# Kernel tuning notes

Hardware: AMD Instinct MI355X
Metric: run time of the kernel (lower is better)

Reference implementation:

```python
import jax, jax.numpy as jnp
import numpy as np

N, E = 50000, 800000
IN, HID, OUT, T = 96, 128, 64, 8
THETA = 0.5


def setup_inputs() -> dict:
    key = jax.random.key(0)
    ks = jax.random.split(key, 8)
    x = jax.random.normal(ks[0], (N, IN), dtype=jnp.float32)
    edge_weight = jax.random.uniform(ks[1], (E,), dtype=jnp.float32)
    W1 = jax.random.normal(ks[2], (IN, HID), dtype=jnp.float32) * (2.0 / np.sqrt(IN + HID))
    W2 = jax.random.normal(ks[3], (HID, OUT), dtype=jnp.float32) * (2.0 / np.sqrt(HID + OUT))
    # Bernoulli(1 - theta) masks, fixed per MC sample (created in __init__)
    mask1 = (jax.random.uniform(ks[4], (T, IN, HID)) < (1.0 - THETA)).astype(jnp.float32)
    mask2 = (jax.random.uniform(ks[5], (T, HID, OUT)) < (1.0 - THETA)).astype(jnp.float32)
    src = jax.random.randint(ks[6], (E,), 0, N, dtype=jnp.int32)
    dst = jax.random.randint(ks[7], (E,), 0, N, dtype=jnp.int32)
    return {"x": x, "edge_weight": edge_weight, "W1": W1, "W2": W2,
            "mask1": mask1, "mask2": mask2, "src": src, "dst": dst}


def _spmm(feat, edge_weight, src, dst, n_nodes):
    # u_mul_e('feat','edge_weight') followed by fn.sum onto dst nodes
    msg = feat[src] * edge_weight[:, None]          # [E, D]
    return jax.ops.segment_sum(msg, dst, num_segments=n_nodes)  # [N, D]


def reference(x, edge_weight, W1, W2, mask1, mask2, src, dst):
    n = x.shape[0]
    # first aggregation is mask-independent -> compute once, share across T samples
    agg1 = _spmm(x, edge_weight, src, dst, n)       # [N, IN]

    def per_sample(m1, m2):
        h = jax.nn.relu(agg1 @ (W1 * m1))           # [N, HID]
        agg2 = _spmm(h, edge_weight, src, dst, n)   # [N, HID]
        return agg2 @ (W2 * m2)                     # [N, OUT]

    # stack of the T per-sample outputs (torch version returns a list)
    return jax.vmap(per_sample)(mask1, mask2)       # [T, N, OUT]
```

## Files before the change

### kernel.cpp

```cpp
#include <hip/hip_runtime.h>

#define N_NODES 50000
#define N_EDGES 800000
#define IN_F 96
#define HID_F 128
#define OUT_F 64
#define T_S 8
#define CAP 48

#define NB_ZERO 196
#define NB_XB 4688
#define NB_WPREP 640
#define NB_PREP (NB_ZERO + NB_XB + NB_WPREP)

typedef __attribute__((ext_vector_type(8))) short short8;
typedef __attribute__((ext_vector_type(4))) float float4v;
typedef __attribute__((ext_vector_type(2))) unsigned uint2v;
typedef __attribute__((ext_vector_type(4))) unsigned uint4v;

__device__ __forceinline__ float bf2f(unsigned short h) {
    unsigned u = ((unsigned)h) << 16;
    float f;
    __builtin_memcpy(&f, &u, 4);
    return f;
}
__device__ __forceinline__ unsigned short f2bf(float f) {
    unsigned u;
    __builtin_memcpy(&u, &f, 4);
    unsigned r = (u + 0x7fffu + ((u >> 16) & 1u)) >> 16;
    return (unsigned short)r;
}
__device__ __forceinline__ float bf_lo(unsigned u) {
    unsigned v = u << 16;
    float f;
    __builtin_memcpy(&f, &v, 4);
    return f;
}
__device__ __forceinline__ float bf_hi(unsigned u) {
    unsigned v = u & 0xffff0000u;
    float f;
    __builtin_memcpy(&f, &v, 4);
    return f;
}

__global__ __launch_bounds__(256) void k_prep(int* __restrict__ cursor,
                                              const float* __restrict__ x,
                                              unsigned short* __restrict__ xb,
                                              const float* __restrict__ W1,
                                              const float* __restrict__ W2,
                                              const float* __restrict__ m1,
                                              const float* __restrict__ m2,
                                              unsigned short* __restrict__ wf) {
    int bid = blockIdx.x;
    if (bid < NB_ZERO) {
        int i = bid * 256 + threadIdx.x;
        if (i < N_NODES) cursor[i] = 0;
        return;
    }
    bid -= NB_ZERO;
    if (bid < NB_XB) {
        int i = bid * 256 + threadIdx.x;
        int idx = i * 4;
        if (idx < N_NODES * IN_F) {
            float4v v = __builtin_nontemporal_load((const float4v*)(x + idx));
            uint2v r;
            r.x = (unsigned)f2bf(v.x) | ((unsigned)f2bf(v.y) << 16);
            r.y = (unsigned)f2bf(v.z) | ((unsigned)f2bf(v.w) << 16);
            *(uint2v*)(xb + idx) = r;
        }
        return;
    }
    bid -= NB_XB;
    {
        int gid = bid * 256 + threadIdx.x;
        if (gid >= T_S * 20480) return;
        int t = gid / 20480;
        int idx = gid % 20480;
        float val;
        if (idx < 12288) {
            int j = idx & 7, lane = (idx >> 3) & 63, fr = idx >> 9;
            int kk = fr >> 3, nt = fr & 7;
            int k = kk * 32 + (lane >> 4) * 8 + j;
            int n = nt * 16 + (lane & 15);
            val = W1[k * HID_F + n] * m1[((size_t)t * IN_F + k) * HID_F + n];
        } else {
            int i2 = idx - 12288;
            int j = i2 & 7, lane = (i2 >> 3) & 63, fr = i2 >> 9;
            int kk = fr >> 2, ot = fr & 3;
            int k = kk * 32 + (lane >> 4) * 8 + j;
            int o = ot * 16 + (lane & 15);
            val = W2[k * OUT_F + o] * m2[((size_t)t * HID_F + k) * OUT_F + o];
        }
        wf[gid] = f2bf(val);
    }
}

__global__ void k_fillB(const int* __restrict__ src, const int* __restrict__ dst,
                        const float* __restrict__ ew, int* __restrict__ cursor,
                        uint2v* __restrict__ bucket) {
    int e = blockIdx.x * 256 + threadIdx.x;
    if (e < N_EDGES) {
        int d = dst[e];
        int pos = atomicAdd(&cursor[d], 1);
        if (pos < CAP) {
            uint2v c;
            c.x = (unsigned)src[e];
            c.y = __float_as_uint(ew[e]);
            __builtin_nontemporal_store(c, &bucket[(size_t)d * CAP + pos]);
        }
    }
}

__global__ __launch_bounds__(256) void k_spmm1(const unsigned short* __restrict__ xb,
                                               const int* __restrict__ cursor,
                                               const uint2v* __restrict__ bucket,
                                               unsigned short* __restrict__ agg1) {
    int wave = threadIdx.x >> 6, lane = threadIdx.x & 63;
    int node = blockIdx.x * 4 + wave;
    int g = lane >> 4, d = lane & 15;
    int dd = (d < 12) ? d : 0;
    int cnt = cursor[node];
    if (cnt > CAP) cnt = CAP;
    int beg = node * CAP, end = beg + cnt;
    const uint4v* xrow = (const uint4v*)xb;
    float acc[8] = {0.f, 0.f, 0.f, 0.f, 0.f, 0.f, 0.f, 0.f};
    int e = beg;
    for (; e + 15 < end; e += 16) {
        uint2v c[4];
        uint4v dt[4];
#pragma unroll
        for (int i = 0; i < 4; i++) c[i] = bucket[e + i * 4 + g];
#pragma unroll
        for (int i = 0; i < 4; i++) dt[i] = xrow[(size_t)c[i].x * 12 + dd];
#pragma unroll
        for (int i = 0; i < 4; i++) {
            float wv = __uint_as_float(c[i].y);
            acc[0] = fmaf(wv, bf_lo(dt[i].x), acc[0]);
            acc[1] = fmaf(wv, bf_hi(dt[i].x), acc[1]);
            acc[2] = fmaf(wv, bf_lo(dt[i].y), acc[2]);
            acc[3] = fmaf(wv, bf_hi(dt[i].y), acc[3]);
            acc[4] = fmaf(wv, bf_lo(dt[i].z), acc[4]);
            acc[5] = fmaf(wv, bf_hi(dt[i].z), acc[5]);
            acc[6] = fmaf(wv, bf_lo(dt[i].w), acc[6]);
            acc[7] = fmaf(wv, bf_hi(dt[i].w), acc[7]);
        }
    }
    for (; e < end; e += 4) {
        int ee = e + g;
        bool ea = ee < end;
        uint2v c = bucket[ea ? ee : beg];
        float wv = ea ? __uint_as_float(c.y) : 0.f;
        uint4v dt = xrow[(size_t)c.x * 12 + dd];
        acc[0] = fmaf(wv, bf_lo(dt.x), acc[0]);
        acc[1] = fmaf(wv, bf_hi(dt.x), acc[1]);
        acc[2] = fmaf(wv, bf_lo(dt.y), acc[2]);
        acc[3] = fmaf(wv, bf_hi(dt.y), acc[3]);
        acc[4] = fmaf(wv, bf_lo(dt.z), acc[4]);
        acc[5] = fmaf(wv, bf_hi(dt.z), acc[5]);
        acc[6] = fmaf(wv, bf_lo(dt.w), acc[6]);
        acc[7] = fmaf(wv, bf_hi(dt.w), acc[7]);
    }
#pragma unroll
    for (int j = 0; j < 8; j++) {
        acc[j] += __shfl_xor(acc[j], 16);
        acc[j] += __shfl_xor(acc[j], 32);
    }
    if (lane < 12) {
        uint4v pk;
        pk.x = (unsigned)f2bf(acc[0]) | ((unsigned)f2bf(acc[1]) << 16);
        pk.y = (unsigned)f2bf(acc[2]) | ((unsigned)f2bf(acc[3]) << 16);
        pk.z = (unsigned)f2bf(acc[4]) | ((unsigned)f2bf(acc[5]) << 16);
        pk.w = (unsigned)f2bf(acc[6]) | ((unsigned)f2bf(acc[7]) << 16);
        ((uint4v*)agg1)[(size_t)node * 12 + d] = pk;
    }
}

__global__ __launch_bounds__(256) void k_gemm(const unsigned short* __restrict__ agg1,
                                              const unsigned short* __restrict__ wfrags,
                                              unsigned short* __restrict__ P, int tBase,
                                              int nodeStride, int tMul) {
    __shared__ __align__(16) unsigned short ldsW[20480];
    __shared__ __align__(16) unsigned short ldsH[4][2176];
    int t = tBase + blockIdx.y;
    const uint4* wsrc = (const uint4*)(wfrags + (size_t)t * 20480);
    uint4* wdst = (uint4*)ldsW;
    for (int i = threadIdx.x; i < 2560; i += 256) wdst[i] = wsrc[i];
    __syncthreads();

    int wave = threadIdx.x >> 6, lane = threadIdx.x & 63;
    int quad = lane >> 4, l15 = lane & 15;

    for (int it = 0; it < 8; it++) {
        int node = blockIdx.x * 512 + it * 64 + wave * 16 + l15;
        bool v = node < N_NODES;

        short8 a[3];
        if (v) {
            const unsigned short* ap = agg1 + (size_t)node * IN_F;
            a[0] = *(const short8*)(ap + 0 * 32 + quad * 8);
            a[1] = *(const short8*)(ap + 1 * 32 + quad * 8);
            a[2] = *(const short8*)(ap + 2 * 32 + quad * 8);
        } else {
            short8 z = {0, 0, 0, 0, 0, 0, 0, 0};
            a[0] = z; a[1] = z; a[2] = z;
        }

        for (int nt = 0; nt < 8; nt++) {
            float4v acc = {0.f, 0.f, 0.f, 0.f};
            for (int kk = 0; kk < 3; kk++) {
                short8 w = *(const short8*)&ldsW[(kk * 8 + nt) * 512 + lane * 8];
                acc = __builtin_amdgcn_mfma_f32_16x16x32_bf16(w, a[kk], acc, 0, 0, 0);
            }
            unsigned h0 = f2bf(fmaxf(acc[0], 0.f));
            unsigned h1 = f2bf(fmaxf(acc[1], 0.f));
            unsigned h2 = f2bf(fmaxf(acc[2], 0.f));
            unsigned h3 = f2bf(fmaxf(acc[3], 0.f));
            uint2 pk;
            pk.x = h0 | (h1 << 16);
            pk.y = h2 | (h3 << 16);
            *(uint2*)&ldsH[wave][l15 * 136 + nt * 16 + quad * 4] = pk;
        }

        short8 hf[4];
        for (int kk = 0; kk < 4; kk++)
            hf[kk] = *(const short8*)&ldsH[wave][l15 * 136 + kk * 32 + quad * 8];

        unsigned short* Pt = P + (size_t)node * nodeStride + (size_t)t * tMul;
        for (int ot = 0; ot < 4; ot++) {
            float4v acc = {0.f, 0.f, 0.f, 0.f};
            for (int kk = 0; kk < 4; kk++) {
                short8 w = *(const short8*)&ldsW[12288 + (kk * 4 + ot) * 512 + lane * 8];
                acc = __builtin_amdgcn_mfma_f32_16x16x32_bf16(w, hf[kk], acc, 0, 0, 0);
            }
            if (v) {
                uint2 pk;
                pk.x = (unsigned)f2bf(acc[0]) | ((unsigned)f2bf(acc[1]) << 16);
                pk.y = (unsigned)f2bf(acc[2]) | ((unsigned)f2bf(acc[3]) << 16);
                *(uint2*)(Pt + ot * 16 + quad * 4) = pk;
            }
        }
    }
}

__global__ __launch_bounds__(256) void k_spmm2(const unsigned short* __restrict__ P,
                                               const int* __restrict__ cursor,
                                               const uint2v* __restrict__ bucket,
                                               float* __restrict__ out) {
    int wave = threadIdx.x >> 6, lane = threadIdx.x & 63;
    int node = blockIdx.x * 4 + wave;
    int cnt = cursor[node];
    if (cnt > CAP) cnt = CAP;
    int beg = node * CAP, end = beg + cnt;
    const uint4v* Pl = (const uint4v*)P + lane;
    float acc[8] = {0.f, 0.f, 0.f, 0.f, 0.f, 0.f, 0.f, 0.f};
    int e = beg;
    for (; e + 7 < end; e += 8) {
        uint2v c[8];
        uint4v d[8];
#pragma unroll
        for (int i = 0; i < 8; i++) c[i] = bucket[e + i];
#pragma unroll
        for (int i = 0; i < 8; i++) d[i] = Pl[(size_t)c[i].x * 64];
#pragma unroll
        for (int i = 0; i < 8; i++) {
            float wv = __uint_as_float(c[i].y);
            acc[0] = fmaf(wv, bf_lo(d[i].x), acc[0]);
            acc[1] = fmaf(wv, bf_hi(d[i].x), acc[1]);
            acc[2] = fmaf(wv, bf_lo(d[i].y), acc[2]);
            acc[3] = fmaf(wv, bf_hi(d[i].y), acc[3]);
            acc[4] = fmaf(wv, bf_lo(d[i].z), acc[4]);
            acc[5] = fmaf(wv, bf_hi(d[i].z), acc[5]);
            acc[6] = fmaf(wv, bf_lo(d[i].w), acc[6]);
            acc[7] = fmaf(wv, bf_hi(d[i].w), acc[7]);
        }
    }
    for (; e + 3 < end; e += 4) {
        uint2v c[4];
        uint4v d[4];
#pragma unroll
        for (int i = 0; i < 4; i++) c[i] = bucket[e + i];
#pragma unroll
        for (int i = 0; i < 4; i++) d[i] = Pl[(size_t)c[i].x * 64];
#pragma unroll
        for (int i = 0; i < 4; i++) {
            float wv = __uint_as_float(c[i].y);
            acc[0] = fmaf(wv, bf_lo(d[i].x), acc[0]);
            acc[1] = fmaf(wv, bf_hi(d[i].x), acc[1]);
            acc[2] = fmaf(wv, bf_lo(d[i].y), acc[2]);
            acc[3] = fmaf(wv, bf_hi(d[i].y), acc[3]);
            acc[4] = fmaf(wv, bf_lo(d[i].z), acc[4]);
            acc[5] = fmaf(wv, bf_hi(d[i].z), acc[5]);
            acc[6] = fmaf(wv, bf_lo(d[i].w), acc[6]);
            acc[7] = fmaf(wv, bf_hi(d[i].w), acc[7]);
        }
    }
    for (; e < end; e++) {
        uint2v c = bucket[e];
        float wv = __uint_as_float(c.y);
        uint4v d = Pl[(size_t)c.x * 64];
        acc[0] = fmaf(wv, bf_lo(d.x), acc[0]);
        acc[1] = fmaf(wv, bf_hi(d.x), acc[1]);
        acc[2] = fmaf(wv, bf_lo(d.y), acc[2]);
        acc[3] = fmaf(wv, bf_hi(d.y), acc[3]);
        acc[4] = fmaf(wv, bf_lo(d.z), acc[4]);
        acc[5] = fmaf(wv, bf_hi(d.z), acc[5]);
        acc[6] = fmaf(wv, bf_lo(d.w), acc[6]);
        acc[7] = fmaf(wv, bf_hi(d.w), acc[7]);
    }
    int t = lane >> 3, o = (lane & 7) * 8;
    float* op = out + ((size_t)t * N_NODES + node) * OUT_F + o;
    float4v v0 = {acc[0], acc[1], acc[2], acc[3]};
    float4v v1 = {acc[4], acc[5], acc[6], acc[7]};
    *(float4v*)op = v0;
    *(float4v*)(op + 4) = v1;
}

__global__ __launch_bounds__(512) void k_spmm2_1t(const unsigned short* __restrict__ P,
                                                  const int* __restrict__ cursor,
                                                  const uint2v* __restrict__ bucket,
                                                  float* __restrict__ out) {
    int node = blockIdx.x * 8 + (threadIdx.x >> 6);
    int o = threadIdx.x & 63;
    if (node >= N_NODES) return;
    int cnt = cursor[node];
    if (cnt > CAP) cnt = CAP;
    int beg = node * CAP, end = beg + cnt;
    const unsigned short* Pt = P + o;
    float a0 = 0.f, a1 = 0.f, a2 = 0.f, a3 = 0.f;
    int e = beg;
    for (; e + 3 < end; e += 4) {
        uint2v c0 = bucket[e];
        uint2v c1 = bucket[e + 1];
        uint2v c2 = bucket[e + 2];
        uint2v c3 = bucket[e + 3];
        a0 += __uint_as_float(c0.y) * bf2f(Pt[(size_t)c0.x * OUT_F]);
        a1 += __uint_as_float(c1.y) * bf2f(Pt[(size_t)c1.x * OUT_F]);
        a2 += __uint_as_float(c2.y) * bf2f(Pt[(size_t)c2.x * OUT_F]);
        a3 += __uint_as_float(c3.y) * bf2f(Pt[(size_t)c3.x * OUT_F]);
    }
    for (; e < end; e++) {
        uint2v c = bucket[e];
        a0 += __uint_as_float(c.y) * bf2f(Pt[(size_t)c.x * OUT_F]);
    }
    out[(size_t)node * OUT_F + o] = a0 + a1 + a2 + a3;
}

extern "C" void kernel_launch(void* const* d_in, const int* in_sizes, int n_in,
                              void* d_out, int out_size, void* d_ws, size_t ws_size,
                              hipStream_t stream) {
    const float* x = (const float*)d_in[0];
    const float* ew = (const float*)d_in[1];
    const float* W1 = (const float*)d_in[2];
    const float* W2 = (const float*)d_in[3];
    const float* m1 = (const float*)d_in[4];
    const float* m2 = (const float*)d_in[5];
    const int* src = (const int*)d_in[6];
    const int* dst = (const int*)d_in[7];
    float* out = (float*)d_out;

    char* w = (char*)d_ws;
    size_t off = 0;
    auto alloc = [&](size_t bytes) -> void* {
        void* p = (void*)(w + off);
        off += (bytes + 255) & ~(size_t)255;
        return p;
    };
    int* cursor = (int*)alloc((size_t)N_NODES * 4);
    uint2v* bucket = (uint2v*)alloc((size_t)N_NODES * CAP * 8);
    unsigned short* agg1 = (unsigned short*)alloc((size_t)N_NODES * IN_F * 2);
    unsigned short* wf = (unsigned short*)alloc((size_t)T_S * 20480 * 2);

    size_t unionBase = off;
    size_t pBytesBatched = (size_t)T_S * N_NODES * OUT_F * 2;
    size_t xbBytes = (size_t)N_NODES * IN_F * 2;
    bool batched = ws_size >= unionBase + (pBytesBatched > xbBytes ? pBytesBatched : xbBytes);
    unsigned short* xb = (unsigned short*)(w + unionBase);
    unsigned short* P = (unsigned short*)(w + unionBase);
    if (!batched) {
        xb = (unsigned short*)(w + unionBase);
        P = (unsigned short*)(w + unionBase + ((xbBytes + 255) & ~(size_t)255));
    }

    k_prep<<<NB_PREP, 256, 0, stream>>>(cursor, x, xb, W1, W2, m1, m2, wf);
    k_fillB<<<N_EDGES / 256, 256, 0, stream>>>(src, dst, ew, cursor, bucket);
    k_spmm1<<<N_NODES / 4, 256, 0, stream>>>(xb, cursor, bucket, agg1);

    if (batched) {
        k_gemm<<<dim3(98, 8), 256, 0, stream>>>(agg1, wf, P, 0, T_S * OUT_F, OUT_F);
        k_spmm2<<<N_NODES / 4, 256, 0, stream>>>(P, cursor, bucket, out);
    } else {
        for (int t = 0; t < T_S; t++) {
            k_gemm<<<dim3(98, 1), 256, 0, stream>>>(agg1, wf, P, t, OUT_F, 0);
            k_spmm2_1t<<<6250, 512, 0, stream>>>(P, cursor, bucket,
                                                 out + (size_t)t * N_NODES * OUT_F);
        }
    }
}
```

Before: 362.7 us.

## Merge prep, bucket fill and first SpMM into one cooperative kernel

Replaces three separate launches (prep, edge bucketing, first aggregation) with a single cooperative kernel of 1024 persistent blocks that uses grid-wide syncs between phases and grid-stride loops. The aim is to remove launch gaps and tail effects between the three front-end stages. In exchange, phases now run on a fixed grid that may use the GPU less fully than the original large grids. Grid syncs add their own cost, and the cooperative launch requires all blocks to be co-resident.

```diff
diff --git a/kernel.cpp b/kernel.cpp
--- a/kernel.cpp
+++ b/kernel.cpp
@@ -1,4 +1,7 @@
 #include <hip/hip_runtime.h>
+#include <hip/hip_cooperative_groups.h>
+
+namespace cg = cooperative_groups;
 
 #define N_NODES 50000
 #define N_EDGES 800000
@@ -8,10 +11,9 @@
 #define T_S 8
 #define CAP 48
 
-#define NB_ZERO 196
-#define NB_XB 4688
-#define NB_WPREP 640
-#define NB_PREP (NB_ZERO + NB_XB + NB_WPREP)
+#define GRID_CO 1024
+#define NTH_CO (GRID_CO * 256)
+#define NWAVE_CO (GRID_CO * 4)
 
 typedef __attribute__((ext_vector_type(8))) short short8;
 typedef __attribute__((ext_vector_type(4))) float float4v;
@@ -43,39 +45,34 @@
     return f;
 }
 
-__global__ __launch_bounds__(256) void k_prep(int* __restrict__ cursor,
-                                              const float* __restrict__ x,
-                                              unsigned short* __restrict__ xb,
-                                              const float* __restrict__ W1,
-                                              const float* __restrict__ W2,
-                                              const float* __restrict__ m1,
-                                              const float* __restrict__ m2,
-                                              unsigned short* __restrict__ wf) {
-    int bid = blockIdx.x;
-    if (bid < NB_ZERO) {
-        int i = bid * 256 + threadIdx.x;
-        if (i < N_NODES) cursor[i] = 0;
-        return;
-    }
-    bid -= NB_ZERO;
-    if (bid < NB_XB) {
-        int i = bid * 256 + threadIdx.x;
+__global__ __launch_bounds__(256, 4) void k_front(int* __restrict__ cursor,
+                                                  const float* __restrict__ x,
+                                                  unsigned short* __restrict__ xb,
+                                                  const float* __restrict__ W1,
+                                                  const float* __restrict__ W2,
+                                                  const float* __restrict__ m1,
+                                                  const float* __restrict__ m2,
+                                                  unsigned short* __restrict__ wf,
+                                                  const int* __restrict__ src,
+                                                  const int* __restrict__ dst,
+                                                  const float* __restrict__ ew,
+                                                  uint2v* __restrict__ bucket,
+                                                  unsigned short* __restrict__ agg1) {
+    cg::grid_group grid = cg::this_grid();
+    int gtid = blockIdx.x * 256 + threadIdx.x;
+
+    if (gtid < N_NODES) cursor[gtid] = 0;
+    for (int i = gtid; i < N_NODES * IN_F / 4; i += NTH_CO) {
         int idx = i * 4;
-        if (idx < N_NODES * IN_F) {
-            float4v v = __builtin_nontemporal_load((const float4v*)(x + idx));
-            uint2v r;
-            r.x = (unsigned)f2bf(v.x) | ((unsigned)f2bf(v.y) << 16);
-            r.y = (unsigned)f2bf(v.z) | ((unsigned)f2bf(v.w) << 16);
-            *(uint2v*)(xb + idx) = r;
-        }
-        return;
-    }
-    bid -= NB_XB;
-    {
-        int gid = bid * 256 + threadIdx.x;
-        if (gid >= T_S * 20480) return;
-        int t = gid / 20480;
-        int idx = gid % 20480;
+        float4v v = __builtin_nontemporal_load((const float4v*)(x + idx));
+        uint2v r;
+        r.x = (unsigned)f2bf(v.x) | ((unsigned)f2bf(v.y) << 16);
+        r.y = (unsigned)f2bf(v.z) | ((unsigned)f2bf(v.w) << 16);
+        *(uint2v*)(xb + idx) = r;
+    }
+    if (gtid < T_S * 20480) {
+        int t = gtid / 20480;
+        int idx = gtid % 20480;
         float val;
         if (idx < 12288) {
             int j = idx & 7, lane = (idx >> 3) & 63, fr = idx >> 9;
@@ -91,15 +88,12 @@
             int o = ot * 16 + (lane & 15);
             val = W2[k * OUT_F + o] * m2[((size_t)t * HID_F + k) * OUT_F + o];
         }
-        wf[gid] = f2bf(val);
-    }
-}
-
-__global__ void k_fillB(const int* __restrict__ src, const int* __restrict__ dst,
-                        const float* __restrict__ ew, int* __restrict__ cursor,
-                        uint2v* __restrict__ bucket) {
-    int e = blockIdx.x * 256 + threadIdx.x;
-    if (e < N_EDGES) {
+        wf[gtid] = f2bf(val);
+    }
+
+    grid.sync();
+
+    for (int e = gtid; e < N_EDGES; e += NTH_CO) {
         int d = dst[e];
         int pos = atomicAdd(&cursor[d], 1);
         if (pos < CAP) {
@@ -109,69 +103,68 @@
             __builtin_nontemporal_store(c, &bucket[(size_t)d * CAP + pos]);
         }
     }
-}
-
-__global__ __launch_bounds__(256) void k_spmm1(const unsigned short* __restrict__ xb,
-                                               const int* __restrict__ cursor,
-                                               const uint2v* __restrict__ bucket,
-                                               unsigned short* __restrict__ agg1) {
-    int wave = threadIdx.x >> 6, lane = threadIdx.x & 63;
-    int node = blockIdx.x * 4 + wave;
+
+    grid.sync();
+
+    int lane = threadIdx.x & 63;
+    int gwave = gtid >> 6;
     int g = lane >> 4, d = lane & 15;
     int dd = (d < 12) ? d : 0;
-    int cnt = cursor[node];
-    if (cnt > CAP) cnt = CAP;
-    int beg = node * CAP, end = beg + cnt;
     const uint4v* xrow = (const uint4v*)xb;
-    float acc[8] = {0.f, 0.f, 0.f, 0.f, 0.f, 0.f, 0.f, 0.f};
-    int e = beg;
-    for (; e + 15 < end; e += 16) {
-        uint2v c[4];
-        uint4v dt[4];
-#pragma unroll
-        for (int i = 0; i < 4; i++) c[i] = bucket[e + i * 4 + g];
-#pragma unroll
-        for (int i = 0; i < 4; i++) dt[i] = xrow[(size_t)c[i].x * 12 + dd];
-#pragma unroll
-        for (int i = 0; i < 4; i++) {
-            float wv = __uint_as_float(c[i].y);
-            acc[0] = fmaf(wv, bf_lo(dt[i].x), acc[0]);
-            acc[1] = fmaf(wv, bf_hi(dt[i].x), acc[1]);
-            acc[2] = fmaf(wv, bf_lo(dt[i].y), acc[2]);
-            acc[3] = fmaf(wv, bf_hi(dt[i].y), acc[3]);
-            acc[4] = fmaf(wv, bf_lo(dt[i].z), acc[4]);
-            acc[5] = fmaf(wv, bf_hi(dt[i].z), acc[5]);
-            acc[6] = fmaf(wv, bf_lo(dt[i].w), acc[6]);
-            acc[7] = fmaf(wv, bf_hi(dt[i].w), acc[7]);
-        }
-    }
-    for (; e < end; e += 4) {
-        int ee = e + g;
-        bool ea = ee < end;
-        uint2v c = bucket[ea ? ee : beg];
-        float wv = ea ? __uint_as_float(c.y) : 0.f;
-        uint4v dt = xrow[(size_t)c.x * 12 + dd];
-        acc[0] = fmaf(wv, bf_lo(dt.x), acc[0]);
-        acc[1] = fmaf(wv, bf_hi(dt.x), acc[1]);
-        acc[2] = fmaf(wv, bf_lo(dt.y), acc[2]);
-        acc[3] = fmaf(wv, bf_hi(dt.y), acc[3]);
-        acc[4] = fmaf(wv, bf_lo(dt.z), acc[4]);
-        acc[5] = fmaf(wv, bf_hi(dt.z), acc[5]);
-        acc[6] = fmaf(wv, bf_lo(dt.w), acc[6]);
-        acc[7] = fmaf(wv, bf_hi(dt.w), acc[7]);
-    }
-#pragma unroll
-    for (int j = 0; j < 8; j++) {
-        acc[j] += __shfl_xor(acc[j], 16);
-        acc[j] += __shfl_xor(acc[j], 32);
-    }
-    if (lane < 12) {
-        uint4v pk;
-        pk.x = (unsigned)f2bf(acc[0]) | ((unsigned)f2bf(acc[1]) << 16);
-        pk.y = (unsigned)f2bf(acc[2]) | ((unsigned)f2bf(acc[3]) << 16);
-        pk.z = (unsigned)f2bf(acc[4]) | ((unsigned)f2bf(acc[5]) << 16);
-        pk.w = (unsigned)f2bf(acc[6]) | ((unsigned)f2bf(acc[7]) << 16);
-        ((uint4v*)agg1)[(size_t)node * 12 + d] = pk;
+    for (int node = gwave; node < N_NODES; node += NWAVE_CO) {
+        int cnt = cursor[node];
+        if (cnt > CAP) cnt = CAP;
+        int beg = node * CAP, end = beg + cnt;
+        float acc[8] = {0.f, 0.f, 0.f, 0.f, 0.f, 0.f, 0.f, 0.f};
+        int e = beg;
+        for (; e + 15 < end; e += 16) {
+            uint2v c[4];
+            uint4v dt[4];
+#pragma unroll
+            for (int i = 0; i < 4; i++) c[i] = bucket[e + i * 4 + g];
+#pragma unroll
+            for (int i = 0; i < 4; i++) dt[i] = xrow[(size_t)c[i].x * 12 + dd];
+#pragma unroll
+            for (int i = 0; i < 4; i++) {
+                float wv = __uint_as_float(c[i].y);
+                acc[0] = fmaf(wv, bf_lo(dt[i].x), acc[0]);
+                acc[1] = fmaf(wv, bf_hi(dt[i].x), acc[1]);
+                acc[2] = fmaf(wv, bf_lo(dt[i].y), acc[2]);
+                acc[3] = fmaf(wv, bf_hi(dt[i].y), acc[3]);
+                acc[4] = fmaf(wv, bf_lo(dt[i].z), acc[4]);
+                acc[5] = fmaf(wv, bf_hi(dt[i].z), acc[5]);
+                acc[6] = fmaf(wv, bf_lo(dt[i].w), acc[6]);
+                acc[7] = fmaf(wv, bf_hi(dt[i].w), acc[7]);
+            }
+        }
+        for (; e < end; e += 4) {
+            int ee = e + g;
+            bool ea = ee < end;
+            uint2v c = bucket[ea ? ee : beg];
+            float wv = ea ? __uint_as_float(c.y) : 0.f;
+            uint4v dt = xrow[(size_t)c.x * 12 + dd];
+            acc[0] = fmaf(wv, bf_lo(dt.x), acc[0]);
+            acc[1] = fmaf(wv, bf_hi(dt.x), acc[1]);
+            acc[2] = fmaf(wv, bf_lo(dt.y), acc[2]);
+            acc[3] = fmaf(wv, bf_hi(dt.y), acc[3]);
+            acc[4] = fmaf(wv, bf_lo(dt.z), acc[4]);
+            acc[5] = fmaf(wv, bf_hi(dt.z), acc[5]);
+            acc[6] = fmaf(wv, bf_lo(dt.w), acc[6]);
+            acc[7] = fmaf(wv, bf_hi(dt.w), acc[7]);
+        }
+#pragma unroll
+        for (int j = 0; j < 8; j++) {
+            acc[j] += __shfl_xor(acc[j], 16);
+            acc[j] += __shfl_xor(acc[j], 32);
+        }
+        if (lane < 12) {
+            uint4v pk;
+            pk.x = (unsigned)f2bf(acc[0]) | ((unsigned)f2bf(acc[1]) << 16);
+            pk.y = (unsigned)f2bf(acc[2]) | ((unsigned)f2bf(acc[3]) << 16);
+            pk.z = (unsigned)f2bf(acc[4]) | ((unsigned)f2bf(acc[5]) << 16);
+            pk.w = (unsigned)f2bf(acc[6]) | ((unsigned)f2bf(acc[7]) << 16);
+            ((uint4v*)agg1)[(size_t)node * 12 + d] = pk;
+        }
     }
 }
 
@@ -381,9 +374,13 @@
         P = (unsigned short*)(w + unionBase + ((xbBytes + 255) & ~(size_t)255));
     }
 
-    k_prep<<<NB_PREP, 256, 0, stream>>>(cursor, x, xb, W1, W2, m1, m2, wf);
-    k_fillB<<<N_EDGES / 256, 256, 0, stream>>>(src, dst, ew, cursor, bucket);
-    k_spmm1<<<N_NODES / 4, 256, 0, stream>>>(xb, cursor, bucket, agg1);
+    {
+        void* args[] = {&cursor, (void*)&x, &xb, (void*)&W1, (void*)&W2,
+                        (void*)&m1, (void*)&m2, &wf, (void*)&src, (void*)&dst,
+                        (void*)&ew, &bucket, &agg1};
+        hipLaunchCooperativeKernel((const void*)k_front, dim3(GRID_CO), dim3(256),
+                                   args, 0, stream);
+    }
 
     if (batched) {
         k_gemm<<<dim3(98, 8), 256, 0, stream>>>(agg1, wf, P, 0, T_S * OUT_F, OUT_F);
```

After: 592.5 us. +63.4%, slower.
